# Kernel optimization log

Hardware: AMD Instinct MI355X
Metric: run time of the kernel (lower is better)

Reference implementation:

```python
import jax, jax.numpy as jnp
import numpy as np

B, C, H, W = 32, 192, 64, 64
O, E, KH, KW = 192, 8, 3, 3


def setup_inputs() -> dict:
    key = jax.random.key(0)
    k1, k2, k3, k4 = jax.random.split(key, 4)
    x = jax.random.normal(k1, (B, C, H, W), dtype=jnp.float32)
    # expert filters stored flattened as in torch: [num_experts, O*(C/groups)*KH*KW]
    expert_weight = jax.random.normal(k2, (E, O * C * KH * KW), dtype=jnp.float32) * 0.02
    routing_w = jax.random.normal(k3, (E, C), dtype=jnp.float32) * 0.05
    routing_b = jax.random.normal(k4, (E,), dtype=jnp.float32) * 0.05
    return {"x": x, "expert_weight": expert_weight, "routing_w": routing_w, "routing_b": routing_b}


def reference(x, expert_weight, routing_w, routing_b):
    # squeeze: global average pool -> routing linear -> sigmoid  [B, E]
    pooled = jnp.mean(x, axis=(2, 3))
    routing = jax.nn.sigmoid(pooled @ routing_w.T + routing_b)
    # per-sample mixed kernels: [B, O, C, KH, KW]
    w = (routing @ expert_weight).reshape(x.shape[0], O, C, KH, KW)
    pad = [(1, 1), (1, 1)]  # static 'same' padding for k=3, s=1, d=1

    def conv_one(xi, wi):
        # xi: [C,H,W], wi: [O,C,KH,KW]
        return jax.lax.conv_general_dilated(
            xi[None], wi, window_strides=(1, 1), padding=pad,
            dimension_numbers=("NCHW", "OIHW", "NCHW"))[0]

    return jax.vmap(conv_one)(x, w)  # [B, O, H, W]
```

## Files before the change

kernel.cpp:

```cpp
#include <hip/hip_runtime.h>
#include <hip/hip_bf16.h>

#define BB 32
#define CC 192
#define HH 64
#define WW 64
#define OO 192
#define EE 8
#define KTOT (CC*9)
#define NSP (HH*WW)
#define EWN (OO*CC*9)

typedef __attribute__((ext_vector_type(8))) __bf16 bf16x8;
typedef __attribute__((ext_vector_type(4))) float f32x4;

__device__ __forceinline__ void gl_lds16(const void* g, void* l) {
    __builtin_amdgcn_global_load_lds(
        (const __attribute__((address_space(1))) unsigned int*)g,
        (__attribute__((address_space(3))) unsigned int*)l, 16, 0, 0);
}

__global__ __launch_bounds__(256) void transpose_pool_kernel(const float* __restrict__ x,
                                                             __bf16* __restrict__ xT,
                                                             float* __restrict__ pooled) {
    const int h = blockIdx.x, b = blockIdx.y;
    __shared__ float T[CC][65];
    const int t = threadIdx.x;
    const float* xb = x + (size_t)b * CC * NSP + h * WW;
#pragma unroll
    for (int i = 0; i < 12; ++i) {
        const int g = i * 256 + t;
        const int c = g >> 4;
        const int w4 = (g & 15) * 4;
        float4 v = *(const float4*)(xb + (size_t)c * NSP + w4);
        T[c][w4 + 0] = v.x; T[c][w4 + 1] = v.y;
        T[c][w4 + 2] = v.z; T[c][w4 + 3] = v.w;
    }
    __syncthreads();
    if (t < CC) {
        float s = 0.f;
#pragma unroll 8
        for (int w = 0; w < WW; ++w) s += T[t][w];
        atomicAdd(pooled + b * CC + t, s);
    }
#pragma unroll
    for (int i = 0; i < 6; ++i) {
        const int ch = i * 256 + t;
        const int w = ch / 24;
        const int cg = ch - w * 24;
        bf16x8 o;
#pragma unroll
        for (int j = 0; j < 8; ++j) o[j] = (__bf16)T[cg * 8 + j][w];
        *(bf16x8*)(xT + (((size_t)b * HH + h) * WW + w) * CC + cg * 8) = o;
    }
}

__global__ __launch_bounds__(256) void mix_kernel(const float* __restrict__ ew,
                                                  const float* __restrict__ pooled,
                                                  const float* __restrict__ rw,
                                                  const float* __restrict__ rb,
                                                  __bf16* __restrict__ wmT) {
    __shared__ float r[4 * EE];
    __shared__ float es[EE * KTOT];
    const int t = threadIdx.x;
    const int o = blockIdx.x;
    const int b0 = blockIdx.y * 4;
    const size_t base = (size_t)o * KTOT;
    for (int u = t; u < EE * (KTOT / 4); u += 256) {
        const int e = u / (KTOT / 4);
        const int s4 = u - e * (KTOT / 4);
        *(float4*)&es[e * KTOT + s4 * 4] =
            *(const float4*)(ew + (size_t)e * EWN + base + s4 * 4);
    }
    {
        const int p = t >> 3, q = t & 7;
        if (p < 32) {
            const int bl = p >> 3, e = p & 7;
            const float* pb = pooled + (b0 + bl) * CC + q * 24;
            const float* we = rw + e * CC + q * 24;
            float s = 0.f;
#pragma unroll
            for (int c = 0; c < 24; ++c) s += pb[c] * we[c];
            s += __shfl_xor(s, 4);
            s += __shfl_xor(s, 2);
            s += __shfl_xor(s, 1);
            if (q == 0) {
                s = s * (1.0f / 4096.0f) + rb[e];
                r[bl * EE + e] = 1.0f / (1.0f + expf(-s));
            }
        }
    }
    __syncthreads();
    for (int i = 0; i < 7; ++i) {
        const int jl = t + 256 * i;
        if (jl >= KTOT) break;
        const int c = jl % 192;
        const int t9 = jl / 192;
        const int s = c * 9 + t9;
        float w8[EE];
#pragma unroll
        for (int e = 0; e < EE; ++e) w8[e] = es[e * KTOT + s];
#pragma unroll
        for (int bi = 0; bi < 4; ++bi) {
            float acc = 0.f;
#pragma unroll
            for (int e = 0; e < EE; ++e) acc += r[bi * EE + e] * w8[e];
            wmT[(size_t)(b0 + bi) * EWN + base + jl] = (__bf16)acc;
        }
    }
}

#define A_ELEMS (192*64)
#define B_ELEMS (128*64)
#define BUFE (A_ELEMS + B_ELEMS)

__global__ __launch_bounds__(512) void conv_kernel(const __bf16* __restrict__ xT,
                                                   const __bf16* __restrict__ wmT,
                                                   const __bf16* __restrict__ zp,
                                                   float* __restrict__ out) {
    extern __shared__ __bf16 smem[];

    const int gid = blockIdx.x;
    const int nid = (gid & 7) * 128 + (gid >> 3);
    const int b  = nid >> 5;
    const int h0 = (nid & 31) * 2;

    const int t = threadIdx.x;
    const int lane = t & 63;
    const int wv = t >> 6;
    const int wr = wv >> 1;
    const int wc = wv & 1;
    const int l15 = lane & 15, lch = lane >> 4;
    const int lrow = lane >> 3;
    const int offB = (((lane & 7) ^ lrow) << 4);

    const char* wmb = (const char*)(wmT + (size_t)b * (OO * KTOT));
    const char* xtb = (const char*)(xT + (size_t)b * (HH * WW * CC));
    const char* zpb = (const char*)zp;

    f32x4 acc[3][4];
#pragma unroll
    for (int mi = 0; mi < 3; ++mi)
#pragma unroll
        for (int ni = 0; ni < 4; ++ni) acc[mi][ni] = (f32x4){0.f, 0.f, 0.f, 0.f};

    auto STAGE = [&](int buf, int step) {
        const int t9 = step / 3;
        const int cc = step - t9 * 3;
        const int kh = t9 / 3;
        const int kw = t9 - kh * 3;
        const int c0 = cc * 64;
        __bf16* As = smem + buf * BUFE;
        __bf16* Bs = As + A_ELEMS;
        const size_t kB = (size_t)step * 128;
#pragma unroll
        for (int i = 0; i < 3; ++i) {
            const int chunk = wv * 3 + i;
            const char* src = wmb + (size_t)(chunk * 8 + lrow) * (KTOT * 2) + kB + offB;
            gl_lds16(src, (void*)(As + chunk * 512));
        }
#pragma unroll
        for (int i = 0; i < 2; ++i) {
            const int chunk = wv * 2 + i;
            const int n = chunk * 8 + lrow;
            const int hl = n >> 6;
            const int w = n & 63;
            const int hp = h0 + hl + kh - 1;
            const int wp = w + kw - 1;
            const bool ok = ((unsigned)hp < (unsigned)HH) && ((unsigned)wp < (unsigned)WW);
            const char* src = ok
                ? xtb + ((size_t)(hp * WW + wp) * CC + c0) * 2 + offB
                : zpb + offB;
            gl_lds16(src, (void*)(Bs + chunk * 512));
        }
    };

    STAGE(0, 0);
    for (int step = 0; step < 27; ++step) {
        const int cur = step & 1;
        if (step + 1 < 27) {
            STAGE(cur ^ 1, step + 1);
            asm volatile("s_waitcnt vmcnt(5)" ::: "memory");
        } else {
            asm volatile("s_waitcnt vmcnt(0)" ::: "memory");
        }
        __builtin_amdgcn_s_barrier();
        __builtin_amdgcn_sched_barrier(0);

        const __bf16* As = smem + cur * BUFE;
        const __bf16* Bs = As + A_ELEMS;
#pragma unroll
        for (int kc = 0; kc < 2; ++kc) {
            bf16x8 a[3], bbf[4];
#pragma unroll
            for (int mi = 0; mi < 3; ++mi) {
                const int r = wr * 48 + mi * 16 + l15;
                const int col = (kc * 64 + lch * 16) ^ ((r & 7) << 4);
                a[mi] = *(const bf16x8*)((const char*)As + r * 128 + col);
            }
#pragma unroll
            for (int ni = 0; ni < 4; ++ni) {
                const int r = wc * 64 + ni * 16 + l15;
                const int col = (kc * 64 + lch * 16) ^ ((r & 7) << 4);
                bbf[ni] = *(const bf16x8*)((const char*)Bs + r * 128 + col);
            }
            __builtin_amdgcn_s_setprio(1);
#pragma unroll
            for (int mi = 0; mi < 3; ++mi)
#pragma unroll
                for (int ni = 0; ni < 4; ++ni)
                    acc[mi][ni] = __builtin_amdgcn_mfma_f32_16x16x32_bf16(
                        a[mi], bbf[ni], acc[mi][ni], 0, 0, 0);
            __builtin_amdgcn_s_setprio(0);
        }
        __builtin_amdgcn_s_barrier();
        __builtin_amdgcn_sched_barrier(0);
    }

    float* ob = out + (size_t)b * OO * NSP + (size_t)(h0 + wc) * WW;
#pragma unroll
    for (int mi = 0; mi < 3; ++mi)
#pragma unroll
        for (int ni = 0; ni < 4; ++ni)
#pragma unroll
            for (int j = 0; j < 4; ++j) {
                const int o = wr * 48 + mi * 16 + lch * 4 + j;
                const int w = ni * 16 + l15;
                __builtin_nontemporal_store(acc[mi][ni][j], &ob[(size_t)o * NSP + w]);
            }
}

extern "C" void kernel_launch(void* const* d_in, const int* in_sizes, int n_in,
                              void* d_out, int out_size, void* d_ws, size_t ws_size,
                              hipStream_t stream) {
    const float* x  = (const float*)d_in[0];
    const float* ew = (const float*)d_in[1];
    const float* rw = (const float*)d_in[2];
    const float* rb = (const float*)d_in[3];
    float* out = (float*)d_out;

    char* ws = (char*)d_ws;
    float*  pooled  = (float*)(ws + 0);
    __bf16* zp      = (__bf16*)(ws + 24576);
    __bf16* xT      = (__bf16*)(ws + 65536);
    __bf16* wmT     = (__bf16*)(ws + 65536 + 50331648);

    hipMemsetAsync(ws, 0, 25600, stream);

    hipFuncSetAttribute((const void*)conv_kernel,
                        hipFuncAttributeMaxDynamicSharedMemorySize, 2 * BUFE * 2);

    hipLaunchKernelGGL(transpose_pool_kernel, dim3(HH, BB), dim3(256), 0, stream,
                       x, xT, pooled);
    hipLaunchKernelGGL(mix_kernel, dim3(OO, 8), dim3(256), 0, stream,
                       ew, pooled, rw, rb, wmT);
    hipLaunchKernelGGL(conv_kernel, dim3(1024), dim3(512), 2 * BUFE * 2, stream,
                       xT, wmT, zp, out);
}
```

Measured before the change: 138.4 us.

## Enlarge conv tile to four output rows and interleave prefetch with MFMA phases

The conv kernel now computes 192 output channels by 256 spatial positions (four image rows) per block, with a 2x4 wave grid where each wave owns 96 channels by 64 positions. The grid is halved to 512 blocks. This halves how often each per-sample weight tile is reloaded. The next stage's global-to-LDS loads are split into pieces issued between four MFMA sub-phases, each separated by barriers, to overlap loads with compute. In exchange the block uses more LDS and twice the accumulator registers, adds barriers, and has fewer blocks to spread across CUs. Output stores also change from nontemporal to plain stores.

```diff
diff --git a/kernel.cpp b/kernel.cpp
--- a/kernel.cpp
+++ b/kernel.cpp
@@ -111,7 +111,7 @@
 }
 
 #define A_ELEMS (192*64)
-#define B_ELEMS (128*64)
+#define B_ELEMS (256*64)
 #define BUFE (A_ELEMS + B_ELEMS)
 
 __global__ __launch_bounds__(512) void conv_kernel(const __bf16* __restrict__ xT,
@@ -121,15 +121,15 @@
     extern __shared__ __bf16 smem[];
 
     const int gid = blockIdx.x;
-    const int nid = (gid & 7) * 128 + (gid >> 3);
-    const int b  = nid >> 5;
-    const int h0 = (nid & 31) * 2;
+    const int nid = (gid & 7) * 64 + (gid >> 3);
+    const int b  = nid >> 4;
+    const int h0 = (nid & 15) * 4;
 
     const int t = threadIdx.x;
     const int lane = t & 63;
     const int wv = t >> 6;
-    const int wr = wv >> 1;
-    const int wc = wv & 1;
+    const int wr  = wv >> 2;
+    const int wcN = wv & 3;
     const int l15 = lane & 15, lch = lane >> 4;
     const int lrow = lane >> 3;
     const int offB = (((lane & 7) ^ lrow) << 4);
@@ -138,95 +138,155 @@
     const char* xtb = (const char*)(xT + (size_t)b * (HH * WW * CC));
     const char* zpb = (const char*)zp;
 
-    f32x4 acc[3][4];
-#pragma unroll
-    for (int mi = 0; mi < 3; ++mi)
+    f32x4 acc[6][4];
+#pragma unroll
+    for (int mi = 0; mi < 6; ++mi)
 #pragma unroll
         for (int ni = 0; ni < 4; ++ni) acc[mi][ni] = (f32x4){0.f, 0.f, 0.f, 0.f};
 
-    auto STAGE = [&](int buf, int step) {
+    auto STAGE_A1 = [&](int buf, int step, int i) {
+        __bf16* As = smem + buf * BUFE;
+        const int chunk = wv * 3 + i;
+        const char* src = wmb + (size_t)(chunk * 8 + lrow) * (KTOT * 2)
+                          + (size_t)step * 128 + offB;
+        gl_lds16(src, (void*)(As + chunk * 512));
+    };
+    auto STAGE_B1 = [&](int buf, int step, int i) {
         const int t9 = step / 3;
         const int cc = step - t9 * 3;
         const int kh = t9 / 3;
         const int kw = t9 - kh * 3;
-        const int c0 = cc * 64;
-        __bf16* As = smem + buf * BUFE;
-        __bf16* Bs = As + A_ELEMS;
-        const size_t kB = (size_t)step * 128;
-#pragma unroll
-        for (int i = 0; i < 3; ++i) {
-            const int chunk = wv * 3 + i;
-            const char* src = wmb + (size_t)(chunk * 8 + lrow) * (KTOT * 2) + kB + offB;
-            gl_lds16(src, (void*)(As + chunk * 512));
-        }
-#pragma unroll
-        for (int i = 0; i < 2; ++i) {
-            const int chunk = wv * 2 + i;
-            const int n = chunk * 8 + lrow;
-            const int hl = n >> 6;
-            const int w = n & 63;
-            const int hp = h0 + hl + kh - 1;
-            const int wp = w + kw - 1;
-            const bool ok = ((unsigned)hp < (unsigned)HH) && ((unsigned)wp < (unsigned)WW);
-            const char* src = ok
-                ? xtb + ((size_t)(hp * WW + wp) * CC + c0) * 2 + offB
-                : zpb + offB;
-            gl_lds16(src, (void*)(Bs + chunk * 512));
-        }
+        __bf16* Bs = smem + buf * BUFE + A_ELEMS;
+        const int chunk = wv * 4 + i;
+        const int n = chunk * 8 + lrow;
+        const int hl = n >> 6;
+        const int w = n & 63;
+        const int hp = h0 + hl + kh - 1;
+        const int wp = w + kw - 1;
+        const bool ok = ((unsigned)hp < (unsigned)HH) && ((unsigned)wp < (unsigned)WW);
+        const char* src = ok
+            ? xtb + ((size_t)(hp * WW + wp) * CC + cc * 64) * 2 + offB
+            : zpb + offB;
+        gl_lds16(src, (void*)(Bs + chunk * 512));
     };
 
-    STAGE(0, 0);
+#pragma unroll
+    for (int i = 0; i < 3; ++i) STAGE_A1(0, 0, i);
+#pragma unroll
+    for (int i = 0; i < 4; ++i) STAGE_B1(0, 0, i);
+
     for (int step = 0; step < 27; ++step) {
         const int cur = step & 1;
-        if (step + 1 < 27) {
-            STAGE(cur ^ 1, step + 1);
-            asm volatile("s_waitcnt vmcnt(5)" ::: "memory");
+        const int nb = cur ^ 1;
+        const bool pf = (step < 26);
+        const char* As = (const char*)(smem + cur * BUFE);
+        const char* Bs = As + A_ELEMS * 2;
+        bf16x8 a[3], bbf[4];
+
+        if (pf) {
+            STAGE_A1(nb, step + 1, 0);
+            STAGE_A1(nb, step + 1, 1);
+            asm volatile("s_waitcnt vmcnt(2)" ::: "memory");
         } else {
             asm volatile("s_waitcnt vmcnt(0)" ::: "memory");
         }
         __builtin_amdgcn_s_barrier();
         __builtin_amdgcn_sched_barrier(0);
-
-        const __bf16* As = smem + cur * BUFE;
-        const __bf16* Bs = As + A_ELEMS;
-#pragma unroll
-        for (int kc = 0; kc < 2; ++kc) {
-            bf16x8 a[3], bbf[4];
-#pragma unroll
-            for (int mi = 0; mi < 3; ++mi) {
-                const int r = wr * 48 + mi * 16 + l15;
-                const int col = (kc * 64 + lch * 16) ^ ((r & 7) << 4);
-                a[mi] = *(const bf16x8*)((const char*)As + r * 128 + col);
-            }
-#pragma unroll
-            for (int ni = 0; ni < 4; ++ni) {
-                const int r = wc * 64 + ni * 16 + l15;
-                const int col = (kc * 64 + lch * 16) ^ ((r & 7) << 4);
-                bbf[ni] = *(const bf16x8*)((const char*)Bs + r * 128 + col);
-            }
-            __builtin_amdgcn_s_setprio(1);
-#pragma unroll
-            for (int mi = 0; mi < 3; ++mi)
-#pragma unroll
-                for (int ni = 0; ni < 4; ++ni)
-                    acc[mi][ni] = __builtin_amdgcn_mfma_f32_16x16x32_bf16(
-                        a[mi], bbf[ni], acc[mi][ni], 0, 0, 0);
-            __builtin_amdgcn_s_setprio(0);
-        }
-        __builtin_amdgcn_s_barrier();
-        __builtin_amdgcn_sched_barrier(0);
-    }
-
-    float* ob = out + (size_t)b * OO * NSP + (size_t)(h0 + wc) * WW;
-#pragma unroll
-    for (int mi = 0; mi < 3; ++mi)
+#pragma unroll
+        for (int ni = 0; ni < 4; ++ni) {
+            const int r = wcN * 64 + ni * 16 + l15;
+            bbf[ni] = *(const bf16x8*)(Bs + r * 128 + ((lch * 16) ^ ((r & 7) << 4)));
+        }
+#pragma unroll
+        for (int i = 0; i < 3; ++i) {
+            const int r = wr * 96 + i * 16 + l15;
+            a[i] = *(const bf16x8*)(As + r * 128 + ((lch * 16) ^ ((r & 7) << 4)));
+        }
+        __builtin_amdgcn_sched_barrier(0);
+        __builtin_amdgcn_s_setprio(1);
+#pragma unroll
+        for (int i = 0; i < 3; ++i)
+#pragma unroll
+            for (int ni = 0; ni < 4; ++ni)
+                acc[i][ni] = __builtin_amdgcn_mfma_f32_16x16x32_bf16(
+                    a[i], bbf[ni], acc[i][ni], 0, 0, 0);
+        __builtin_amdgcn_s_setprio(0);
+        __builtin_amdgcn_s_barrier();
+        __builtin_amdgcn_sched_barrier(0);
+
+#pragma unroll
+        for (int i = 0; i < 3; ++i) {
+            const int r = wr * 96 + (3 + i) * 16 + l15;
+            a[i] = *(const bf16x8*)(As + r * 128 + ((lch * 16) ^ ((r & 7) << 4)));
+        }
+        if (pf) { STAGE_A1(nb, step + 1, 2); STAGE_B1(nb, step + 1, 0); }
+        __builtin_amdgcn_sched_barrier(0);
+        __builtin_amdgcn_s_barrier();
+        __builtin_amdgcn_s_setprio(1);
+#pragma unroll
+        for (int i = 0; i < 3; ++i)
+#pragma unroll
+            for (int ni = 0; ni < 4; ++ni)
+                acc[3 + i][ni] = __builtin_amdgcn_mfma_f32_16x16x32_bf16(
+                    a[i], bbf[ni], acc[3 + i][ni], 0, 0, 0);
+        __builtin_amdgcn_s_setprio(0);
+        __builtin_amdgcn_s_barrier();
+        __builtin_amdgcn_sched_barrier(0);
+
+#pragma unroll
+        for (int ni = 0; ni < 4; ++ni) {
+            const int r = wcN * 64 + ni * 16 + l15;
+            bbf[ni] = *(const bf16x8*)(Bs + r * 128 + ((64 + lch * 16) ^ ((r & 7) << 4)));
+        }
+#pragma unroll
+        for (int i = 0; i < 3; ++i) {
+            const int r = wr * 96 + i * 16 + l15;
+            a[i] = *(const bf16x8*)(As + r * 128 + ((64 + lch * 16) ^ ((r & 7) << 4)));
+        }
+        if (pf) { STAGE_B1(nb, step + 1, 1); STAGE_B1(nb, step + 1, 2); }
+        __builtin_amdgcn_sched_barrier(0);
+        __builtin_amdgcn_s_barrier();
+        __builtin_amdgcn_s_setprio(1);
+#pragma unroll
+        for (int i = 0; i < 3; ++i)
+#pragma unroll
+            for (int ni = 0; ni < 4; ++ni)
+                acc[i][ni] = __builtin_amdgcn_mfma_f32_16x16x32_bf16(
+                    a[i], bbf[ni], acc[i][ni], 0, 0, 0);
+        __builtin_amdgcn_s_setprio(0);
+        __builtin_amdgcn_s_barrier();
+        __builtin_amdgcn_sched_barrier(0);
+
+#pragma unroll
+        for (int i = 0; i < 3; ++i) {
+            const int r = wr * 96 + (3 + i) * 16 + l15;
+            a[i] = *(const bf16x8*)(As + r * 128 + ((64 + lch * 16) ^ ((r & 7) << 4)));
+        }
+        if (pf) { STAGE_B1(nb, step + 1, 3); }
+        __builtin_amdgcn_sched_barrier(0);
+        __builtin_amdgcn_s_barrier();
+        __builtin_amdgcn_s_setprio(1);
+#pragma unroll
+        for (int i = 0; i < 3; ++i)
+#pragma unroll
+            for (int ni = 0; ni < 4; ++ni)
+                acc[3 + i][ni] = __builtin_amdgcn_mfma_f32_16x16x32_bf16(
+                    a[i], bbf[ni], acc[3 + i][ni], 0, 0, 0);
+        __builtin_amdgcn_s_setprio(0);
+        __builtin_amdgcn_s_barrier();
+        __builtin_amdgcn_sched_barrier(0);
+    }
+
+    float* ob = out + (size_t)b * OO * NSP + (size_t)(h0 + wcN) * WW;
+#pragma unroll
+    for (int mi = 0; mi < 6; ++mi)
 #pragma unroll
         for (int ni = 0; ni < 4; ++ni)
 #pragma unroll
             for (int j = 0; j < 4; ++j) {
-                const int o = wr * 48 + mi * 16 + lch * 4 + j;
+                const int o = wr * 96 + mi * 16 + lch * 4 + j;
                 const int w = ni * 16 + l15;
-                __builtin_nontemporal_store(acc[mi][ni][j], &ob[(size_t)o * NSP + w]);
+                ob[(size_t)o * NSP + w] = acc[mi][ni][j];
             }
 }
 
@@ -254,6 +314,6 @@
                        x, xT, pooled);
     hipLaunchKernelGGL(mix_kernel, dim3(OO, 8), dim3(256), 0, stream,
                        ew, pooled, rw, rb, wmT);
-    hipLaunchKernelGGL(conv_kernel, dim3(1024), dim3(512), 2 * BUFE * 2, stream,
+    hipLaunchKernelGGL(conv_kernel, dim3(512), dim3(512), 2 * BUFE * 2, stream,
                        xT, wmT, zp, out);
 }
```

Result: slower. 151.7 us (+9.7%).
